# Kernel tuning notes

Hardware: AMD Instinct MI355X
Metric: run time of the kernel (lower is better)

Reference implementation:

```python
import jax, jax.numpy as jnp
import numpy as np

B, N, D, K, L, H, DFF = 2048, 64, 256, 32, 2, 8, 1024
TEMP = 10.0
EPS = 1e-10


def _ln(x, g, b):
    m = jnp.mean(x, -1, keepdims=True)
    v = jnp.mean((x - m) ** 2, -1, keepdims=True)
    return (x - m) * jax.lax.rsqrt(v + 1e-5) * g + b


def _mha(x, Wqkv, bqkv, Wo, bo):
    b, n, d = x.shape
    dh = d // H
    qkv = x @ Wqkv.T + bqkv                      # [b,n,3d]
    q, k, v = jnp.split(qkv, 3, axis=-1)
    q = q.reshape(b, n, H, dh)
    k = k.reshape(b, n, H, dh)
    v = v.reshape(b, n, H, dh)
    att = jnp.einsum('bqhd,bkhd->bhqk', q, k) / np.float32(np.sqrt(dh))
    att = jax.nn.softmax(att, axis=-1)
    o = jnp.einsum('bhqk,bkhd->bqhd', att, v).reshape(b, n, d)
    return o @ Wo.T + bo


def _encoder(x, Wqkv, bqkv, Wo, bo, ln1_g, ln1_b, ln2_g, ln2_b, W1, b1, W2, b2):
    # torch TransformerEncoder, norm_first=False (post-LN), dropout=0
    for l in range(L):
        x = _ln(x + _mha(x, Wqkv[l], bqkv[l], Wo[l], bo[l]), ln1_g[l], ln1_b[l])
        h = jax.nn.relu(x @ W1[l].T + b1[l]) @ W2[l].T + b2[l]
        x = _ln(x + h, ln2_g[l], ln2_b[l])
    return x


def _cluster_probs_from_emb(emb, mus):
    # ||x - tanh(mu)||^2 via expansion to avoid the [B,N,K,D] intermediate
    mt = jnp.tanh(mus)                                       # [K,D]
    d2 = (jnp.sum(emb ** 2, -1)[..., None]
          - 2.0 * jnp.einsum('bnd,kd->bnk', emb, mt)
          + jnp.sum(mt ** 2, -1))                            # [B,N,K]
    e = jnp.exp(-d2 / TEMP)
    return e / jnp.sum(e, -1, keepdims=True)


def _forward(input_series, init_logits, transition_logits,
             Wqkv, bqkv, Wo, bo, ln1_g, ln1_b, ln2_g, ln2_b,
             W1, b1, W2, b2, mus):
    prob_pi = jax.nn.softmax(init_logits, axis=0)            # [K]
    prob_A = jax.nn.softmax(transition_logits, axis=1)       # [K,K]
    emb_all = _encoder(input_series, Wqkv, bqkv, Wo, bo,
                       ln1_g, ln1_b, ln2_g, ln2_b, W1, b1, W2, b2)
    logits_all = _cluster_probs_from_emb(emb_all, mus)       # [B,N,K]

    log_emit = jnp.log(logits_all + EPS)                     # [B,N,K]
    lt0 = jax.nn.softmax(jnp.log(prob_pi + EPS)[None, :] + log_emit[:, 0], axis=1)

    def step(lt, le):
        lt = jax.nn.softmax(jnp.log(lt @ prob_A + EPS) + le, axis=1)
        return lt, lt

    _, rest = jax.lax.scan(step, lt0, jnp.swapaxes(log_emit[:, 1:], 0, 1))
    cluster_probs = jnp.concatenate([lt0[:, None], jnp.swapaxes(rest, 0, 1)], axis=1)
    entropy_loss = -jnp.mean(jnp.sum(cluster_probs * jnp.log(cluster_probs + EPS), -1))
    return cluster_probs, emb_all, prob_pi, prob_A, entropy_loss


def setup_inputs() -> dict:
    key = jax.random.key(0)
    ks = jax.random.split(key, 10)
    s = jnp.float32(0.02)
    return {
        'input_series': jax.random.normal(ks[0], (B, N, D), jnp.float32),
        'init_logits': jax.random.normal(ks[1], (K,), jnp.float32),
        'transition_logits': jax.random.normal(ks[2], (K, K), jnp.float32),
        'Wqkv': jax.random.normal(ks[3], (L, 3 * D, D), jnp.float32) * s,
        'bqkv': jnp.zeros((L, 3 * D), jnp.float32),
        'Wo': jax.random.normal(ks[4], (L, D, D), jnp.float32) * s,
        'bo': jnp.zeros((L, D), jnp.float32),
        'ln1_g': jnp.ones((L, D), jnp.float32),
        'ln1_b': jnp.zeros((L, D), jnp.float32),
        'ln2_g': jnp.ones((L, D), jnp.float32),
        'ln2_b': jnp.zeros((L, D), jnp.float32),
        'W1': jax.random.normal(ks[5], (L, DFF, D), jnp.float32) * s,
        'b1': jnp.zeros((L, DFF), jnp.float32),
        'W2': jax.random.normal(ks[6], (L, D, DFF), jnp.float32) * s,
        'b2': jnp.zeros((L, D), jnp.float32),
        'mus': jax.random.normal(ks[7], (K, D), jnp.float32),
    }


def reference(input_series, init_logits, transition_logits, Wqkv, bqkv, Wo, bo,
              ln1_g, ln1_b, ln2_g, ln2_b, W1, b1, W2, b2, mus):
    return _forward(input_series, init_logits, transition_logits, Wqkv, bqkv,
                    Wo, bo, ln1_g, ln1_b, ln2_g, ln2_b, W1, b1, W2, b2, mus)
```

## Files before the change

kernel.cpp:

```cpp
#include <hip/hip_runtime.h>

#define BB   2048
#define NNX  64
#define DD   256
#define KKC  32
#define LLN  2
#define HHN  8
#define DHH  32
#define DFFN 1024
#define BNT  (BB*NNX)

typedef short s16x8 __attribute__((ext_vector_type(8)));
typedef float f32x4 __attribute__((ext_vector_type(4)));

#define GLOAD_LDS16(gp, lp) __builtin_amdgcn_global_load_lds( \
    (const __attribute__((address_space(1))) void*)(gp),      \
    (__attribute__((address_space(3))) void*)(lp), 16, 0, 0)

#define WAITVM4() asm volatile("s_waitcnt vmcnt(4)" ::: "memory")
#define WAITVM0() asm volatile("s_waitcnt vmcnt(0)" ::: "memory")
#define WAITLGKM0() do { asm volatile("s_waitcnt lgkmcnt(0)" ::: "memory"); \
                         __builtin_amdgcn_sched_barrier(0); } while (0)
#define SBAR() __builtin_amdgcn_s_barrier()

__device__ __forceinline__ unsigned short f2bf(float f) {
  unsigned int u = __float_as_uint(f);
  u += 0x7fffu + ((u >> 16) & 1u);
  return (unsigned short)(u >> 16);
}
__device__ __forceinline__ float bf2f(unsigned short u) {
  return __uint_as_float(((unsigned int)u) << 16);
}

__device__ __forceinline__ unsigned char f2fp8(float f) {
  unsigned u = __float_as_uint(f);
  unsigned lsb = (u >> 20) & 1u;
  u += 0x7FFFFu + lsb;
  int e = (int)((u >> 23) & 255u) - 120;
  if (e <= 0) {
    int q = (int)(f * 512.f + 0.5f);
    return (unsigned char)q;
  }
  if (e > 15) return 0x7E;
  return (unsigned char)((e << 3) | ((u >> 20) & 7u));
}
__device__ __forceinline__ unsigned char f2fp8s(float f) {
  unsigned s = __float_as_uint(f) >> 31;
  float a = fminf(fabsf(f), 448.f);
  return (unsigned char)((s << 7) | f2fp8(a));
}
__device__ __forceinline__ unsigned char p2fp8(float f) {
  unsigned u = __float_as_uint(f);
  u += 0x7FFFFu + ((u >> 20) & 1u);
  int e = (int)((u >> 23) & 255u) - 120;
  if (e <= 0) return 0;
  return (unsigned char)((e << 3) | ((u >> 20) & 7u));
}

__global__ __launch_bounds__(256) void cvt_kernel(const float4* __restrict__ src,
                                                  ushort4* __restrict__ dst, int n4) {
  int i = blockIdx.x * 256 + threadIdx.x;
  int st = gridDim.x * 256;
  for (; i < n4; i += st) {
    float4 v = src[i];
    ushort4 o;
    o.x = f2bf(v.x); o.y = f2bf(v.y); o.z = f2bf(v.z); o.w = f2bf(v.w);
    dst[i] = o;
  }
}

__global__ __launch_bounds__(256) void cvtw_kernel(const float4* __restrict__ wq, ushort4* __restrict__ dq,
                                                   const float4* __restrict__ wo, ushort4* __restrict__ dov,
                                                   const float4* __restrict__ w1, ushort4* __restrict__ d1,
                                                   const float4* __restrict__ w2, uchar4* __restrict__ d2) {
  const int n0 = 98304, n1 = 32768, n2 = 131072, n3 = 131072;
  int i = blockIdx.x * 256 + threadIdx.x;
  int st = gridDim.x * 256;
  for (; i < n0 + n1 + n2 + n3; i += st) {
    int j = i;
    if (j < n0) {
      float4 v = wq[j];
      dq[j] = (ushort4){f2bf(v.x), f2bf(v.y), f2bf(v.z), f2bf(v.w)};
    } else if ((j -= n0) < n1) {
      float4 v = wo[j];
      dov[j] = (ushort4){f2bf(v.x), f2bf(v.y), f2bf(v.z), f2bf(v.w)};
    } else if ((j -= n1) < n2) {
      float4 v = w1[j];
      d1[j] = (ushort4){f2bf(v.x), f2bf(v.y), f2bf(v.z), f2bf(v.w)};
    } else {
      j -= n2;
      float4 v = w2[j];
      d2[j] = (uchar4){f2fp8s(v.x * 64.f), f2fp8s(v.y * 64.f),
                       f2fp8s(v.z * 64.f), f2fp8s(v.w * 64.f)};
    }
  }
}

__global__ void mtpi_kernel(const float* __restrict__ mus, unsigned short* __restrict__ mtb,
                            float* __restrict__ mtn,
                            const float* __restrict__ il, const float* __restrict__ tl,
                            float* __restrict__ d_pi, float* __restrict__ d_A,
                            float* __restrict__ d_ent) {
  int lane = threadIdx.x;
  if (blockIdx.x == 0) {
    if (lane < 32) {
      float acc = 0.f;
      for (int d = 0; d < 256; d++) {
        float t = tanhf(mus[lane * 256 + d]);
        mtb[lane * 264 + d] = f2bf(t);
        acc += t * t;
      }
      mtn[lane] = acc;
    }
  } else {
    if (lane == 0) *d_ent = 0.f;
    if (lane < 32) {
      float v = il[lane];
      float mx = v;
      #pragma unroll
      for (int off = 16; off; off >>= 1) mx = fmaxf(mx, __shfl_xor(mx, off, 32));
      float e = expf(v - mx), sm = e;
      #pragma unroll
      for (int off = 16; off; off >>= 1) sm += __shfl_xor(sm, off, 32);
      d_pi[lane] = e / sm;
      for (int r = 0; r < 32; r++) {
        float a = tl[r * 32 + lane];
        float m2 = a;
        #pragma unroll
        for (int off = 16; off; off >>= 1) m2 = fmaxf(m2, __shfl_xor(m2, off, 32));
        float e2 = expf(a - m2), s2 = e2;
        #pragma unroll
        for (int off = 16; off; off >>= 1) s2 += __shfl_xor(s2, off, 32);
        d_A[r * 32 + lane] = e2 / s2;
      }
    }
  }
}

template <int EPI>
__global__ __launch_bounds__(256, 4) void gemm_nt(const unsigned short* __restrict__ A,
                                                  const unsigned short* __restrict__ Bw,
                                                  const float* __restrict__ bias,
                                                  void* __restrict__ outp,
                                                  int N, int K, int nx) {
  __shared__ unsigned short lds[16384];
  const int t = threadIdx.x;
  const int bid = blockIdx.x, nwg = gridDim.x;
  const int wg = (bid & 7) * (nwg >> 3) + (bid >> 3);
  const int m0 = (wg / nx) << 7;
  const int n0 = (wg % nx) << 7;
  const int lane = t & 63, w = t >> 6;
  const int wm = w >> 1, wn = w & 1;
  const int lr = lane & 15, lk = lane >> 4;

  const int r0 = t >> 2, sg = t & 3;
  const int s0 = sg ^ ((r0 >> 1) & 3);
  const int r1 = r0 + 64;
  const int s1 = sg ^ ((r1 >> 1) & 3);
  const int aoff0 = (m0 + r0) * K + s0 * 8;
  const int aoff1 = (m0 + r1) * K + s1 * 8;
  const int boff0 = (n0 + r0) * K + s0 * 8;
  const int boff1 = (n0 + r1) * K + s1 * 8;

#define STAGE(buf, k0) do {                                    \
    char* la = (char*)lds + (buf) * 16384;                     \
    GLOAD_LDS16(A + aoff0 + (k0), la + t * 16);                \
    GLOAD_LDS16(A + aoff1 + (k0), la + 4096 + t * 16);         \
    GLOAD_LDS16(Bw + boff0 + (k0), la + 8192 + t * 16);        \
    GLOAD_LDS16(Bw + boff1 + (k0), la + 12288 + t * 16);       \
  } while (0)

  f32x4 acc[4][4];
  #pragma unroll
  for (int i = 0; i < 4; i++)
    #pragma unroll
    for (int j = 0; j < 4; j++) acc[i][j] = (f32x4)(0.f);

  const int ra = wm * 64 + lr, rb = wn * 64 + lr;
  const int sla = lk ^ ((ra >> 1) & 3), slb = lk ^ ((rb >> 1) & 3);

  const int NT = K >> 5;
  STAGE(0, 0);
  STAGE(1, 32);
  WAITVM4();
  SBAR();

  int c = 0;
  for (int kt = 0; kt < NT; kt++) {
    s16x8 af[4], bf[4];
    {
      const unsigned short* ua = lds + c * 8192;
      const unsigned short* ub = ua + 4096;
      #pragma unroll
      for (int mf = 0; mf < 4; mf++)
        af[mf] = *(const s16x8*)&ua[(ra + mf * 16) * 32 + sla * 8];
      #pragma unroll
      for (int nf = 0; nf < 4; nf++)
        bf[nf] = *(const s16x8*)&ub[(rb + nf * 16) * 32 + slb * 8];
    }
    __builtin_amdgcn_s_setprio(1);
    #pragma unroll
    for (int mf = 0; mf < 4; mf++)
      #pragma unroll
      for (int nf = 0; nf < 4; nf++)
        acc[mf][nf] = __builtin_amdgcn_mfma_f32_16x16x32_bf16(af[mf], bf[nf], acc[mf][nf], 0, 0, 0);
    __builtin_amdgcn_s_setprio(0);
    SBAR();
    if (kt < NT - 2) {
      STAGE(c, (kt + 2) << 5);
      WAITVM4();
    } else if (kt == NT - 2) {
      WAITVM0();
    }
    SBAR();
    c ^= 1;
  }
#undef STAGE

  #pragma unroll
  for (int nf = 0; nf < 4; nf++) {
    int col = n0 + wn * 64 + nf * 16 + lr;
    float bv = bias[col];
    #pragma unroll
    for (int mf = 0; mf < 4; mf++)
      #pragma unroll
      for (int r = 0; r < 4; r++) {
        int row = m0 + wm * 64 + mf * 16 + lk * 4 + r;
        size_t o = (size_t)row * N + col;
        float v = acc[mf][nf][r] + bv;
        if (EPI == 0) {
          ((unsigned short*)outp)[o] = f2bf(v);
        } else if (EPI == 1) {
          float hh = fminf(fmaxf(v, 0.f) * 8.f, 448.f);
          ((unsigned char*)outp)[o] = f2fp8(hh);
        } else {
          ((unsigned char*)outp)[o] = f2fp8s(v * 32.f);
        }
      }
  }
}

template <bool WR32>
__global__ __launch_bounds__(512) void gemm_ln(const unsigned short* __restrict__ A,
                                               const unsigned short* __restrict__ Bw,
                                               const float* __restrict__ bias,
                                               const unsigned short* __restrict__ res,
                                               const float* __restrict__ g,
                                               const float* __restrict__ bta,
                                               unsigned short* __restrict__ xb,
                                               float* __restrict__ x32,
                                               int K) {
  __shared__ unsigned short As[128 * 64];
  __shared__ unsigned short Bs[256 * 64];
  __shared__ float stats[2][128][4];
  const int t = threadIdx.x;
  const int nwg = gridDim.x;
  const int bid = blockIdx.x;
  const int wg = (bid & 7) * (nwg >> 3) + (bid >> 3);
  const int m0 = wg << 7;

  const int lane = t & 63, w = t >> 6;
  const int wm = w >> 2, wn = w & 3;
  const int lr = lane & 15, lk = lane >> 4;

  size_t aoff[2], boff[4];
  #pragma unroll
  for (int p = 0; p < 2; p++) {
    int u = p * 512 + t;
    int row = u >> 3, sp = u & 7;
    int seg = sp ^ (((row >> 2) & 1) << 1);
    aoff[p] = (size_t)(m0 + row) * K + seg * 8;
  }
  #pragma unroll
  for (int p = 0; p < 4; p++) {
    int u = p * 512 + t;
    int row = u >> 3, sp = u & 7;
    int seg = sp ^ (((row >> 2) & 1) << 1);
    boff[p] = (size_t)row * K + seg * 8;
  }

  f32x4 acc[4][4];
  #pragma unroll
  for (int i = 0; i < 4; i++)
    #pragma unroll
    for (int j = 0; j < 4; j++) acc[i][j] = (f32x4)(0.f);

  for (int k0 = 0; k0 < K; k0 += 64) {
    #pragma unroll
    for (int p = 0; p < 2; p++)
      GLOAD_LDS16(A + aoff[p] + k0, (char*)As + (p * 512 + t) * 16);
    #pragma unroll
    for (int p = 0; p < 4; p++)
      GLOAD_LDS16(Bw + boff[p] + k0, (char*)Bs + (p * 512 + t) * 16);
    __syncthreads();
    #pragma unroll
    for (int z = 0; z < 2; z++) {
      s16x8 af[4], bfr[4];
      #pragma unroll
      for (int mf = 0; mf < 4; mf++) {
        int row = wm * 64 + mf * 16 + lr;
        int cc = (z * 4 + lk) ^ (((row >> 2) & 1) << 1);
        af[mf] = *(const s16x8*)&As[row * 64 + cc * 8];
      }
      #pragma unroll
      for (int nf = 0; nf < 4; nf++) {
        int row = wn * 64 + nf * 16 + lr;
        int cc = (z * 4 + lk) ^ (((row >> 2) & 1) << 1);
        bfr[nf] = *(const s16x8*)&Bs[row * 64 + cc * 8];
      }
      #pragma unroll
      for (int mf = 0; mf < 4; mf++)
        #pragma unroll
        for (int nf = 0; nf < 4; nf++)
          acc[mf][nf] = __builtin_amdgcn_mfma_f32_16x16x32_bf16(af[mf], bfr[nf], acc[mf][nf], 0, 0, 0);
    }
    __syncthreads();
  }

  float bv[4];
  #pragma unroll
  for (int nf = 0; nf < 4; nf++) bv[nf] = bias[wn * 64 + nf * 16 + lr];

  #pragma unroll
  for (int mf = 0; mf < 4; mf++) {
    #pragma unroll
    for (int r = 0; r < 4; r++) {
      int grow = m0 + wm * 64 + mf * 16 + lk * 4 + r;
      float s = 0.f, q = 0.f;
      #pragma unroll
      for (int nf = 0; nf < 4; nf++) {
        int col = wn * 64 + nf * 16 + lr;
        float v = acc[mf][nf][r] + bv[nf] + bf2f(res[(size_t)grow * 256 + col]);
        acc[mf][nf][r] = v;
        s += v; q += v * v;
      }
      #pragma unroll
      for (int off = 1; off < 16; off <<= 1) { s += __shfl_xor(s, off); q += __shfl_xor(q, off); }
      if (lr == 0) {
        int lrow = wm * 64 + mf * 16 + lk * 4 + r;
        stats[0][lrow][wn] = s;
        stats[1][lrow][wn] = q;
      }
    }
  }
  __syncthreads();

  float gv[4], bbv[4];
  #pragma unroll
  for (int nf = 0; nf < 4; nf++) {
    int col = wn * 64 + nf * 16 + lr;
    gv[nf] = g[col]; bbv[nf] = bta[col];
  }
  #pragma unroll
  for (int mf = 0; mf < 4; mf++) {
    #pragma unroll
    for (int r = 0; r < 4; r++) {
      int lrow = wm * 64 + mf * 16 + lk * 4 + r;
      int grow = m0 + lrow;
      float s4 = stats[0][lrow][0] + stats[0][lrow][1] + stats[0][lrow][2] + stats[0][lrow][3];
      float q4 = stats[1][lrow][0] + stats[1][lrow][1] + stats[1][lrow][2] + stats[1][lrow][3];
      float mean = s4 * (1.f / 256.f);
      float var = q4 * (1.f / 256.f) - mean * mean;
      float rs = rsqrtf(var + 1e-5f);
      #pragma unroll
      for (int nf = 0; nf < 4; nf++) {
        int col = wn * 64 + nf * 16 + lr;
        float val = (acc[mf][nf][r] - mean) * rs * gv[nf] + bbv[nf];
        xb[(size_t)grow * 256 + col] = f2bf(val);
        if (WR32) x32[(size_t)grow * 256 + col] = val;
      }
    }
  }
}

template <bool WR32>
__global__ __launch_bounds__(512) void gemm_ln_fp8(const unsigned char* __restrict__ A,
                                                   const unsigned char* __restrict__ Bw,
                                                   const float* __restrict__ bias,
                                                   const unsigned short* __restrict__ res,
                                                   const float* __restrict__ g,
                                                   const float* __restrict__ bta,
                                                   unsigned short* __restrict__ xb,
                                                   float* __restrict__ x32,
                                                   int K) {
  __shared__ unsigned char lds8[24576];
  float* stats = (float*)lds8;
  const int t = threadIdx.x;
  const int nwg = gridDim.x;
  const int bid = blockIdx.x;
  const int wg = (bid & 7) * (nwg >> 3) + (bid >> 3);
  const int m0 = wg << 7;

  const int lane = t & 63, w = t >> 6;
  const int wm = w >> 2, wn = w & 3;
  const int lr = lane & 15, lk = lane >> 4;

  const int auu = t >> 8, arow = (t >> 1) & 127, asg = t & 1;
  const size_t aoff = (size_t)(m0 + arow) * K + auu * 32 + asg * 16;
  size_t boff[2];
  #pragma unroll
  for (int p = 0; p < 2; p++) {
    int idx = p * 512 + t;
    int buu = idx >> 9, brow = (idx >> 1) & 255, bsg = idx & 1;
    boff[p] = (size_t)brow * K + buu * 32 + bsg * 16;
  }

  f32x4 acc[4][4];
  #pragma unroll
  for (int i = 0; i < 4; i++)
    #pragma unroll
    for (int j = 0; j < 4; j++) acc[i][j] = (f32x4)(0.f);

  for (int k0 = 0; k0 < K; k0 += 64) {
    GLOAD_LDS16(A + aoff + k0, (char*)lds8 + t * 16);
    GLOAD_LDS16(Bw + boff[0] + k0, (char*)lds8 + 8192 + t * 16);
    GLOAD_LDS16(Bw + boff[1] + k0, (char*)lds8 + 16384 + t * 16);
    __syncthreads();
    #pragma unroll
    for (int kk = 0; kk < 2; kk++) {
      long long af[4], bf[4];
      #pragma unroll
      for (int mf = 0; mf < 4; mf++)
        af[mf] = *(const long long*)&lds8[kk * 4096 + (wm * 64 + mf * 16 + lr) * 32 + lk * 8];
      #pragma unroll
      for (int nf = 0; nf < 4; nf++)
        bf[nf] = *(const long long*)&lds8[8192 + kk * 8192 + (wn * 64 + nf * 16 + lr) * 32 + lk * 8];
      #pragma unroll
      for (int mf = 0; mf < 4; mf++)
        #pragma unroll
        for (int nf = 0; nf < 4; nf++)
          acc[mf][nf] = __builtin_amdgcn_mfma_f32_16x16x32_fp8_fp8(af[mf], bf[nf], acc[mf][nf], 0, 0, 0);
    }
    __syncthreads();
  }

  const float isc = 1.f / 512.f;
  float bv[4];
  #pragma unroll
  for (int nf = 0; nf < 4; nf++) bv[nf] = bias[wn * 64 + nf * 16 + lr];

  #pragma unroll
  for (int mf = 0; mf < 4; mf++) {
    #pragma unroll
    for (int r = 0; r < 4; r++) {
      int grow = m0 + wm * 64 + mf * 16 + lk * 4 + r;
      float s = 0.f, q = 0.f;
      #pragma unroll
      for (int nf = 0; nf < 4; nf++) {
        int col = wn * 64 + nf * 16 + lr;
        float v = acc[mf][nf][r] * isc + bv[nf] + bf2f(res[(size_t)grow * 256 + col]);
        acc[mf][nf][r] = v;
        s += v; q += v * v;
      }
      #pragma unroll
      for (int off = 1; off < 16; off <<= 1) { s += __shfl_xor(s, off); q += __shfl_xor(q, off); }
      if (lr == 0) {
        int lrow = wm * 64 + mf * 16 + lk * 4 + r;
        stats[lrow * 4 + wn] = s;
        stats[512 + lrow * 4 + wn] = q;
      }
    }
  }
  __syncthreads();

  float gv[4], bbv[4];
  #pragma unroll
  for (int nf = 0; nf < 4; nf++) {
    int col = wn * 64 + nf * 16 + lr;
    gv[nf] = g[col]; bbv[nf] = bta[col];
  }
  #pragma unroll
  for (int mf = 0; mf < 4; mf++) {
    #pragma unroll
    for (int r = 0; r < 4; r++) {
      int lrow = wm * 64 + mf * 16 + lk * 4 + r;
      int grow = m0 + lrow;
      float s4 = stats[lrow * 4 + 0] + stats[lrow * 4 + 1] + stats[lrow * 4 + 2] + stats[lrow * 4 + 3];
      float q4 = stats[512 + lrow * 4 + 0] + stats[512 + lrow * 4 + 1]
               + stats[512 + lrow * 4 + 2] + stats[512 + lrow * 4 + 3];
      float mean = s4 * (1.f / 256.f);
      float var = q4 * (1.f / 256.f) - mean * mean;
      float rs = rsqrtf(var + 1e-5f);
      #pragma unroll
      for (int nf = 0; nf < 4; nf++) {
        int col = wn * 64 + nf * 16 + lr;
        float val = (acc[mf][nf][r] - mean) * rs * gv[nf] + bbv[nf];
        xb[(size_t)grow * 256 + col] = f2bf(val);
        if (WR32) x32[(size_t)grow * 256 + col] = val;
      }
    }
  }
}

__global__ __launch_bounds__(64) void attn_kernel(const unsigned char* __restrict__ qkv,
                                                  unsigned short* __restrict__ ob) {
  __shared__ unsigned char al[7168];
  unsigned char* qs = al;
  unsigned char* ks = al + 2048;
  unsigned char* vs = al + 4096;
  unsigned char* vt = al;
  unsigned char* ps = al + 2304;
  const int bh = blockIdx.x;
  const int b = bh >> 3, h = bh & 7;
  const int lane = threadIdx.x;
  const int lr = lane & 15, lk = lane >> 4;

  #pragma unroll
  for (int p = 0; p < 2; p++) {
    int u = lane + p * 64;
    int row = u >> 1, seg = u & 1;
    size_t gb = (size_t)(b * 64 + row) * 768 + h * 32 + seg * 16;
    GLOAD_LDS16(qkv + gb, (char*)al + u * 16);
    GLOAD_LDS16(qkv + gb + 256, (char*)al + 2048 + u * 16);
    GLOAD_LDS16(qkv + gb + 512, (char*)al + 4096 + u * 16);
  }
  __syncthreads();

  long long aq[4], bk[4], vchunk[4];
  #pragma unroll
  for (int mi = 0; mi < 4; mi++)
    aq[mi] = *(const long long*)&qs[(mi * 16 + lr) * 32 + lk * 8];
  #pragma unroll
  for (int nj = 0; nj < 4; nj++)
    bk[nj] = *(const long long*)&ks[(nj * 16 + lr) * 32 + lk * 8];
  const int vrow = lane >> 2, vcs = (lane & 3) * 8;
  #pragma unroll
  for (int q = 0; q < 4; q++)
    vchunk[q] = *(const long long*)&vs[(q * 16 + vrow) * 32 + vcs];
  WAITLGKM0();

  #pragma unroll
  for (int q = 0; q < 4; q++) {
    unsigned long long vv = (unsigned long long)vchunk[q];
    #pragma unroll
    for (int j = 0; j < 8; j++)
      vt[(vcs + j) * 72 + q * 16 + vrow] = (unsigned char)(vv >> (8 * j));
  }

  f32x4 s[4][4];
  #pragma unroll
  for (int i = 0; i < 4; i++)
    #pragma unroll
    for (int j = 0; j < 4; j++) s[i][j] = (f32x4)(0.f);
  #pragma unroll
  for (int mi = 0; mi < 4; mi++)
    #pragma unroll
    for (int nj = 0; nj < 4; nj++)
      s[mi][nj] = __builtin_amdgcn_mfma_f32_16x16x32_fp8_fp8(aq[mi], bk[nj], s[mi][nj], 0, 0, 0);

  const float scale = 0.17677669529663687f / 1024.f;
  #pragma unroll
  for (int mi = 0; mi < 4; mi++) {
    #pragma unroll
    for (int r = 0; r < 4; r++) {
      float t0 = s[mi][0][r] * scale, t1 = s[mi][1][r] * scale;
      float t2 = s[mi][2][r] * scale, t3 = s[mi][3][r] * scale;
      float mx = fmaxf(fmaxf(t0, t1), fmaxf(t2, t3));
      #pragma unroll
      for (int off = 8; off; off >>= 1) mx = fmaxf(mx, __shfl_xor(mx, off, 16));
      float e0 = expf(t0 - mx), e1 = expf(t1 - mx), e2 = expf(t2 - mx), e3 = expf(t3 - mx);
      float sm = e0 + e1 + e2 + e3;
      #pragma unroll
      for (int off = 8; off; off >>= 1) sm += __shfl_xor(sm, off, 16);
      float inv = 128.f / sm;
      int prow = mi * 16 + lk * 4 + r;
      ps[prow * 72 + lr + 0]  = p2fp8(e0 * inv);
      ps[prow * 72 + lr + 16] = p2fp8(e1 * inv);
      ps[prow * 72 + lr + 32] = p2fp8(e2 * inv);
      ps[prow * 72 + lr + 48] = p2fp8(e3 * inv);
    }
  }
  WAITLGKM0();

  f32x4 oacc[4][2];
  #pragma unroll
  for (int i = 0; i < 4; i++) { oacc[i][0] = (f32x4)(0.f); oacc[i][1] = (f32x4)(0.f); }
  #pragma unroll
  for (int kk = 0; kk < 2; kk++) {
    long long bv[2];
    #pragma unroll
    for (int nf = 0; nf < 2; nf++)
      bv[nf] = *(const long long*)&vt[(nf * 16 + lr) * 72 + kk * 32 + lk * 8];
    #pragma unroll
    for (int mi = 0; mi < 4; mi++) {
      long long ap = *(const long long*)&ps[(mi * 16 + lr) * 72 + kk * 32 + lk * 8];
      #pragma unroll
      for (int nf = 0; nf < 2; nf++)
        oacc[mi][nf] = __builtin_amdgcn_mfma_f32_16x16x32_fp8_fp8(ap, bv[nf], oacc[mi][nf], 0, 0, 0);
    }
  }
  const float osc = 1.f / 4096.f;
  #pragma unroll
  for (int mi = 0; mi < 4; mi++)
    #pragma unroll
    for (int nf = 0; nf < 2; nf++)
      #pragma unroll
      for (int r = 0; r < 4; r++) {
        int tok = mi * 16 + lk * 4 + r;
        int c = nf * 16 + lr;
        ob[(size_t)(b * 64 + tok) * 256 + h * 32 + c] = f2bf(oacc[mi][nf][r] * osc);
      }
}

__global__ __launch_bounds__(256) void cluster_kernel(const unsigned short* __restrict__ xb,
                                                      const unsigned short* __restrict__ mtb,
                                                      const float* __restrict__ mtn,
                                                      float* __restrict__ log_emit) {
  __shared__ unsigned short ms[32 * 264];
  const int t = threadIdx.x;
  for (int i = t; i < 2112; i += 256)
    ((uint2*)ms)[i] = ((const uint2*)mtb)[i];
  const int lane = t & 63, w = t >> 6;
  const int lr = lane & 15, lk = lane >> 4;
  const float mtn0 = mtn[lr], mtn1 = mtn[16 + lr];
  __syncthreads();

  const size_t tok0 = (size_t)blockIdx.x * 256 + (size_t)w * 64;
  f32x4 s[4][2];
  #pragma unroll
  for (int i = 0; i < 4; i++) { s[i][0] = (f32x4)(0.f); s[i][1] = (f32x4)(0.f); }

  #pragma unroll
  for (int kk = 0; kk < 8; kk++) {
    s16x8 bf0 = *(const s16x8*)&ms[lr * 264 + lk * 8 + kk * 32];
    s16x8 bf1 = *(const s16x8*)&ms[(16 + lr) * 264 + lk * 8 + kk * 32];
    #pragma unroll
    for (int mi = 0; mi < 4; mi++) {
      s16x8 af = *(const s16x8*)&xb[(tok0 + mi * 16 + lr) * 256 + lk * 8 + kk * 32];
      s[mi][0] = __builtin_amdgcn_mfma_f32_16x16x32_bf16(af, bf0, s[mi][0], 0, 0, 0);
      s[mi][1] = __builtin_amdgcn_mfma_f32_16x16x32_bf16(af, bf1, s[mi][1], 0, 0, 0);
    }
  }

  #pragma unroll
  for (int mi = 0; mi < 4; mi++) {
    #pragma unroll
    for (int r = 0; r < 4; r++) {
      float l0 = (2.f * s[mi][0][r] - mtn0) * 0.1f;
      float l1 = (2.f * s[mi][1][r] - mtn1) * 0.1f;
      float mx = fmaxf(l0, l1);
      #pragma unroll
      for (int off = 8; off; off >>= 1) mx = fmaxf(mx, __shfl_xor(mx, off, 16));
      float e0 = expf(l0 - mx), e1 = expf(l1 - mx);
      float sm = e0 + e1;
      #pragma unroll
      for (int off = 8; off; off >>= 1) sm += __shfl_xor(sm, off, 16);
      float inv = 1.f / sm;
      size_t row = tok0 + mi * 16 + lk * 4 + r;
      log_emit[row * 32 + lr]      = logf(e0 * inv + 1e-10f);
      log_emit[row * 32 + 16 + lr] = logf(e1 * inv + 1e-10f);
    }
  }
}

__global__ __launch_bounds__(256) void scan_kernel(const float* __restrict__ log_emit,
                                                   const float* __restrict__ pi,
                                                   const float* __restrict__ A,
                                                   float* __restrict__ cp,
                                                   float* __restrict__ ent) {
  const int g = threadIdx.x >> 5, j = threadIdx.x & 31;
  const int batch = blockIdx.x * 8 + g;
  float regA[32];
  #pragma unroll
  for (int i = 0; i < 32; i++) regA[i] = A[i * 32 + j];
  const float* le = log_emit + (size_t)batch * 64 * 32;
  float* cpo = cp + (size_t)batch * 64 * 32;

  float u = logf(pi[j] + 1e-10f) + le[j];
  float mx = u;
  #pragma unroll
  for (int off = 16; off; off >>= 1) mx = fmaxf(mx, __shfl_xor(mx, off, 32));
  float e = expf(u - mx), sm = e;
  #pragma unroll
  for (int off = 16; off; off >>= 1) sm += __shfl_xor(sm, off, 32);
  float p = e / sm;
  cpo[j] = p;
  float enta = p * logf(p + 1e-10f);

  for (int n = 1; n < 64; n++) {
    float tt = 0.f;
    #pragma unroll
    for (int i = 0; i < 32; i++) tt += __shfl(p, i, 32) * regA[i];
    u = logf(tt + 1e-10f) + le[n * 32 + j];
    mx = u;
    #pragma unroll
    for (int off = 16; off; off >>= 1) mx = fmaxf(mx, __shfl_xor(mx, off, 32));
    e = expf(u - mx); sm = e;
    #pragma unroll
    for (int off = 16; off; off >>= 1) sm += __shfl_xor(sm, off, 32);
    p = e / sm;
    cpo[n * 32 + j] = p;
    enta += p * logf(p + 1e-10f);
  }
  #pragma unroll
  for (int off = 16; off; off >>= 1) enta += __shfl_xor(enta, off, 32);
  if (j == 0) atomicAdd(ent, -enta * (1.f / (2048.f * 64.f)));
}

extern "C" void kernel_launch(void* const* d_in, const int* in_sizes, int n_in,
                              void* d_out, int out_size, void* d_ws, size_t ws_size,
                              hipStream_t stream) {
  const float* input = (const float*)d_in[0];
  const float* init_logits = (const float*)d_in[1];
  const float* trans = (const float*)d_in[2];
  const float* Wqkv = (const float*)d_in[3];
  const float* bqkv = (const float*)d_in[4];
  const float* Wo = (const float*)d_in[5];
  const float* bo = (const float*)d_in[6];
  const float* ln1g = (const float*)d_in[7];
  const float* ln1b = (const float*)d_in[8];
  const float* ln2g = (const float*)d_in[9];
  const float* ln2b = (const float*)d_in[10];
  const float* W1 = (const float*)d_in[11];
  const float* b1 = (const float*)d_in[12];
  const float* W2 = (const float*)d_in[13];
  const float* b2 = (const float*)d_in[14];
  const float* mus = (const float*)d_in[15];

  float* out = (float*)d_out;
  float* cp = out;
  float* x = out + 4194304;
  float* d_pi = out + 37748736;
  float* d_A = out + 37748768;
  float* d_ent = out + 37749792;

  char* ws = (char*)d_ws;
  unsigned char* qkv = (unsigned char*)ws;
  unsigned char* hb = (unsigned char*)ws;
  float* log_emit = (float*)ws;
  unsigned short* ob = (unsigned short*)(ws + 268435456ull);
  unsigned short* xb = (unsigned short*)(ws + 335544320ull);
  unsigned short* wq_b = (unsigned short*)(ws + 402653184ull);
  unsigned short* wo_b = (unsigned short*)(ws + 402653184ull + 786432ull);
  unsigned short* w1_b = (unsigned short*)(ws + 402653184ull + 1048576ull);
  unsigned char* w2_f = (unsigned char*)(ws + 402653184ull + 2097152ull);
  unsigned short* mtb = (unsigned short*)(ws + 402653184ull + 3145728ull);
  float* mtn = (float*)(ws + 402653184ull + 3178496ull);

  cvt_kernel<<<2048, 256, 0, stream>>>((const float4*)input, (ushort4*)xb, BNT * 256 / 4);
  cvtw_kernel<<<512, 256, 0, stream>>>((const float4*)Wqkv, (ushort4*)wq_b,
                                       (const float4*)Wo, (ushort4*)wo_b,
                                       (const float4*)W1, (ushort4*)w1_b,
                                       (const float4*)W2, (uchar4*)w2_f);
  mtpi_kernel<<<2, 64, 0, stream>>>(mus, mtb, mtn, init_logits, trans, d_pi, d_A, d_ent);

  for (int l = 0; l < 2; l++) {
    gemm_nt<2><<<6144, 256, 0, stream>>>(xb, wq_b + l * 196608, bqkv + l * 768,
                                         qkv, 768, 256, 6);
    attn_kernel<<<16384, 64, 0, stream>>>(qkv, ob);
    gemm_ln<false><<<1024, 512, 0, stream>>>(ob, wo_b + l * 65536, bo + l * 256,
                                             xb, ln1g + l * 256, ln1b + l * 256,
                                             xb, nullptr, 256);
    gemm_nt<1><<<8192, 256, 0, stream>>>(xb, w1_b + l * 262144, b1 + l * 1024,
                                         hb, 1024, 256, 8);
    if (l == LLN - 1)
      gemm_ln_fp8<true><<<1024, 512, 0, stream>>>(hb, w2_f + l * 262144, b2 + l * 256,
                                                  xb, ln2g + l * 256, ln2b + l * 256,
                                                  xb, x, 1024);
    else
      gemm_ln_fp8<false><<<1024, 512, 0, stream>>>(hb, w2_f + l * 262144, b2 + l * 256,
                                                   xb, ln2g + l * 256, ln2b + l * 256,
                                                   xb, nullptr, 1024);
  }

  cluster_kernel<<<512, 256, 0, stream>>>(xb, mtb, mtn, log_emit);
  scan_kernel<<<256, 256, 0, stream>>>(log_emit, d_pi, d_A, cp, d_ent);
}
```

Before: 1.075 ms.

## Fuse cluster and scan kernels, merge setup kernels, pack four attention heads per block

```diff
diff --git a/kernel.cpp b/kernel.cpp
--- a/kernel.cpp
+++ b/kernel.cpp
@@ -72,10 +72,52 @@
 __global__ __launch_bounds__(256) void cvtw_kernel(const float4* __restrict__ wq, ushort4* __restrict__ dq,
                                                    const float4* __restrict__ wo, ushort4* __restrict__ dov,
                                                    const float4* __restrict__ w1, ushort4* __restrict__ d1,
-                                                   const float4* __restrict__ w2, uchar4* __restrict__ d2) {
+                                                   const float4* __restrict__ w2, uchar4* __restrict__ d2,
+                                                   const float* __restrict__ mus, unsigned short* __restrict__ mtb,
+                                                   float* __restrict__ mtn,
+                                                   const float* __restrict__ il, const float* __restrict__ tl,
+                                                   float* __restrict__ d_pi, float* __restrict__ d_A,
+                                                   float* __restrict__ d_ent) {
+  if (blockIdx.x >= 512) {
+    int lane = threadIdx.x;
+    if (blockIdx.x == 512) {
+      if (lane < 32) {
+        float acc = 0.f;
+        for (int d = 0; d < 256; d++) {
+          float t = tanhf(mus[lane * 256 + d]);
+          mtb[lane * 264 + d] = f2bf(t);
+          acc += t * t;
+        }
+        mtn[lane] = acc;
+      }
+    } else {
+      if (lane == 0) *d_ent = 0.f;
+      if (lane < 32) {
+        float v = il[lane];
+        float mx = v;
+        #pragma unroll
+        for (int off = 16; off; off >>= 1) mx = fmaxf(mx, __shfl_xor(mx, off, 32));
+        float e = expf(v - mx), sm = e;
+        #pragma unroll
+        for (int off = 16; off; off >>= 1) sm += __shfl_xor(sm, off, 32);
+        d_pi[lane] = e / sm;
+        for (int r = 0; r < 32; r++) {
+          float a = tl[r * 32 + lane];
+          float m2 = a;
+          #pragma unroll
+          for (int off = 16; off; off >>= 1) m2 = fmaxf(m2, __shfl_xor(m2, off, 32));
+          float e2 = expf(a - m2), s2 = e2;
+          #pragma unroll
+          for (int off = 16; off; off >>= 1) s2 += __shfl_xor(s2, off, 32);
+          d_A[r * 32 + lane] = e2 / s2;
+        }
+      }
+    }
+    return;
+  }
   const int n0 = 98304, n1 = 32768, n2 = 131072, n3 = 131072;
   int i = blockIdx.x * 256 + threadIdx.x;
-  int st = gridDim.x * 256;
+  int st = 512 * 256;
   for (; i < n0 + n1 + n2 + n3; i += st) {
     int j = i;
     if (j < n0) {
@@ -92,47 +134,6 @@
       float4 v = w2[j];
       d2[j] = (uchar4){f2fp8s(v.x * 64.f), f2fp8s(v.y * 64.f),
                        f2fp8s(v.z * 64.f), f2fp8s(v.w * 64.f)};
-    }
-  }
-}
-
-__global__ void mtpi_kernel(const float* __restrict__ mus, unsigned short* __restrict__ mtb,
-                            float* __restrict__ mtn,
-                            const float* __restrict__ il, const float* __restrict__ tl,
-                            float* __restrict__ d_pi, float* __restrict__ d_A,
-                            float* __restrict__ d_ent) {
-  int lane = threadIdx.x;
-  if (blockIdx.x == 0) {
-    if (lane < 32) {
-      float acc = 0.f;
-      for (int d = 0; d < 256; d++) {
-        float t = tanhf(mus[lane * 256 + d]);
-        mtb[lane * 264 + d] = f2bf(t);
-        acc += t * t;
-      }
-      mtn[lane] = acc;
-    }
-  } else {
-    if (lane == 0) *d_ent = 0.f;
-    if (lane < 32) {
-      float v = il[lane];
-      float mx = v;
-      #pragma unroll
-      for (int off = 16; off; off >>= 1) mx = fmaxf(mx, __shfl_xor(mx, off, 32));
-      float e = expf(v - mx), sm = e;
-      #pragma unroll
-      for (int off = 16; off; off >>= 1) sm += __shfl_xor(sm, off, 32);
-      d_pi[lane] = e / sm;
-      for (int r = 0; r < 32; r++) {
-        float a = tl[r * 32 + lane];
-        float m2 = a;
-        #pragma unroll
-        for (int off = 16; off; off >>= 1) m2 = fmaxf(m2, __shfl_xor(m2, off, 32));
-        float e2 = expf(a - m2), s2 = e2;
-        #pragma unroll
-        for (int off = 16; off; off >>= 1) s2 += __shfl_xor(s2, off, 32);
-        d_A[r * 32 + lane] = e2 / s2;
-      }
     }
   }
 }
@@ -492,17 +493,19 @@
   }
 }
 
-__global__ __launch_bounds__(64) void attn_kernel(const unsigned char* __restrict__ qkv,
-                                                  unsigned short* __restrict__ ob) {
-  __shared__ unsigned char al[7168];
-  unsigned char* qs = al;
-  unsigned char* ks = al + 2048;
-  unsigned char* vs = al + 4096;
-  unsigned char* vt = al;
-  unsigned char* ps = al + 2304;
-  const int bh = blockIdx.x;
+__global__ __launch_bounds__(256) void attn_kernel(const unsigned char* __restrict__ qkv,
+                                                   unsigned short* __restrict__ ob) {
+  __shared__ unsigned char al[28672];
+  const int wv = threadIdx.x >> 6;
+  unsigned char* wb = al + wv * 7168;
+  unsigned char* qs = wb;
+  unsigned char* ks = wb + 2048;
+  unsigned char* vs = wb + 4096;
+  unsigned char* vt = wb;
+  unsigned char* ps = wb + 2304;
+  const int bh = blockIdx.x * 4 + wv;
   const int b = bh >> 3, h = bh & 7;
-  const int lane = threadIdx.x;
+  const int lane = threadIdx.x & 63;
   const int lr = lane & 15, lk = lane >> 4;
 
   #pragma unroll
@@ -510,9 +513,9 @@
     int u = lane + p * 64;
     int row = u >> 1, seg = u & 1;
     size_t gb = (size_t)(b * 64 + row) * 768 + h * 32 + seg * 16;
-    GLOAD_LDS16(qkv + gb, (char*)al + u * 16);
-    GLOAD_LDS16(qkv + gb + 256, (char*)al + 2048 + u * 16);
-    GLOAD_LDS16(qkv + gb + 512, (char*)al + 4096 + u * 16);
+    GLOAD_LDS16(qkv + gb, (char*)wb + u * 16);
+    GLOAD_LDS16(qkv + gb + 256, (char*)wb + 2048 + u * 16);
+    GLOAD_LDS16(qkv + gb + 512, (char*)wb + 4096 + u * 16);
   }
   __syncthreads();
 
@@ -602,11 +605,15 @@
       }
 }
 
-__global__ __launch_bounds__(256) void cluster_kernel(const unsigned short* __restrict__ xb,
-                                                      const unsigned short* __restrict__ mtb,
-                                                      const float* __restrict__ mtn,
-                                                      float* __restrict__ log_emit) {
+__global__ __launch_bounds__(256) void cluster_scan_kernel(const unsigned short* __restrict__ xb,
+                                                           const unsigned short* __restrict__ mtb,
+                                                           const float* __restrict__ mtn,
+                                                           const float* __restrict__ pi,
+                                                           const float* __restrict__ Atr,
+                                                           float* __restrict__ cp,
+                                                           float* __restrict__ ent) {
   __shared__ unsigned short ms[32 * 264];
+  __shared__ float les[4][64][32];
   const int t = threadIdx.x;
   for (int i = t; i < 2112; i += 256)
     ((uint2*)ms)[i] = ((const uint2*)mtb)[i];
@@ -646,55 +653,50 @@
       #pragma unroll
       for (int off = 8; off; off >>= 1) sm += __shfl_xor(sm, off, 16);
       float inv = 1.f / sm;
-      size_t row = tok0 + mi * 16 + lk * 4 + r;
-      log_emit[row * 32 + lr]      = logf(e0 * inv + 1e-10f);
-      log_emit[row * 32 + 16 + lr] = logf(e1 * inv + 1e-10f);
-    }
-  }
-}
-
-__global__ __launch_bounds__(256) void scan_kernel(const float* __restrict__ log_emit,
-                                                   const float* __restrict__ pi,
-                                                   const float* __restrict__ A,
-                                                   float* __restrict__ cp,
-                                                   float* __restrict__ ent) {
-  const int g = threadIdx.x >> 5, j = threadIdx.x & 31;
-  const int batch = blockIdx.x * 8 + g;
-  float regA[32];
-  #pragma unroll
-  for (int i = 0; i < 32; i++) regA[i] = A[i * 32 + j];
-  const float* le = log_emit + (size_t)batch * 64 * 32;
-  float* cpo = cp + (size_t)batch * 64 * 32;
-
-  float u = logf(pi[j] + 1e-10f) + le[j];
-  float mx = u;
-  #pragma unroll
-  for (int off = 16; off; off >>= 1) mx = fmaxf(mx, __shfl_xor(mx, off, 32));
-  float e = expf(u - mx), sm = e;
-  #pragma unroll
-  for (int off = 16; off; off >>= 1) sm += __shfl_xor(sm, off, 32);
-  float p = e / sm;
-  cpo[j] = p;
-  float enta = p * logf(p + 1e-10f);
-
-  for (int n = 1; n < 64; n++) {
-    float tt = 0.f;
-    #pragma unroll
-    for (int i = 0; i < 32; i++) tt += __shfl(p, i, 32) * regA[i];
-    u = logf(tt + 1e-10f) + le[n * 32 + j];
-    mx = u;
+      int row = mi * 16 + lk * 4 + r;
+      les[w][row][lr]      = logf(e0 * inv + 1e-10f);
+      les[w][row][16 + lr] = logf(e1 * inv + 1e-10f);
+    }
+  }
+
+  if (lane < 32) {
+    const int j = lane;
+    const int batch = blockIdx.x * 4 + w;
+    float regA[32];
+    #pragma unroll
+    for (int i = 0; i < 32; i++) regA[i] = Atr[i * 32 + j];
+    float* cpo = cp + (size_t)batch * 64 * 32;
+
+    float u = logf(pi[j] + 1e-10f) + les[w][0][j];
+    float mx = u;
     #pragma unroll
     for (int off = 16; off; off >>= 1) mx = fmaxf(mx, __shfl_xor(mx, off, 32));
-    e = expf(u - mx); sm = e;
+    float e = expf(u - mx), sm = e;
     #pragma unroll
     for (int off = 16; off; off >>= 1) sm += __shfl_xor(sm, off, 32);
-    p = e / sm;
-    cpo[n * 32 + j] = p;
-    enta += p * logf(p + 1e-10f);
-  }
-  #pragma unroll
-  for (int off = 16; off; off >>= 1) enta += __shfl_xor(enta, off, 32);
-  if (j == 0) atomicAdd(ent, -enta * (1.f / (2048.f * 64.f)));
+    float p = e / sm;
+    cpo[j] = p;
+    float enta = p * logf(p + 1e-10f);
+
+    for (int n = 1; n < 64; n++) {
+      float tt = 0.f;
+      #pragma unroll
+      for (int i = 0; i < 32; i++) tt += __shfl(p, i, 32) * regA[i];
+      u = logf(tt + 1e-10f) + les[w][n][j];
+      mx = u;
+      #pragma unroll
+      for (int off = 16; off; off >>= 1) mx = fmaxf(mx, __shfl_xor(mx, off, 32));
+      e = expf(u - mx); sm = e;
+      #pragma unroll
+      for (int off = 16; off; off >>= 1) sm += __shfl_xor(sm, off, 32);
+      p = e / sm;
+      cpo[n * 32 + j] = p;
+      enta += p * logf(p + 1e-10f);
+    }
+    #pragma unroll
+    for (int off = 16; off; off >>= 1) enta += __shfl_xor(enta, off, 32);
+    if (j == 0) atomicAdd(ent, -enta * (1.f / (2048.f * 64.f)));
+  }
 }
 
 extern "C" void kernel_launch(void* const* d_in, const int* in_sizes, int n_in,
@@ -727,7 +729,6 @@
   char* ws = (char*)d_ws;
   unsigned char* qkv = (unsigned char*)ws;
   unsigned char* hb = (unsigned char*)ws;
-  float* log_emit = (float*)ws;
   unsigned short* ob = (unsigned short*)(ws + 268435456ull);
   unsigned short* xb = (unsigned short*)(ws + 335544320ull);
   unsigned short* wq_b = (unsigned short*)(ws + 402653184ull);
@@ -738,16 +739,17 @@
   float* mtn = (float*)(ws + 402653184ull + 3178496ull);
 
   cvt_kernel<<<2048, 256, 0, stream>>>((const float4*)input, (ushort4*)xb, BNT * 256 / 4);
-  cvtw_kernel<<<512, 256, 0, stream>>>((const float4*)Wqkv, (ushort4*)wq_b,
+  cvtw_kernel<<<514, 256, 0, stream>>>((const float4*)Wqkv, (ushort4*)wq_b,
                                        (const float4*)Wo, (ushort4*)wo_b,
                                        (const float4*)W1, (ushort4*)w1_b,
-                                       (const float4*)W2, (uchar4*)w2_f);
-  mtpi_kernel<<<2, 64, 0, stream>>>(mus, mtb, mtn, init_logits, trans, d_pi, d_A, d_ent);
+                                       (const float4*)W2, (uchar4*)w2_f,
+                                       mus, mtb, mtn,
+                                       init_logits, trans, d_pi, d_A, d_ent);
 
   for (int l = 0; l < 2; l++) {
     gemm_nt<2><<<6144, 256, 0, stream>>>(xb, wq_b + l * 196608, bqkv + l * 768,
                                          qkv, 768, 256, 6);
-    attn_kernel<<<16384, 64, 0, stream>>>(qkv, ob);
+    attn_kernel<<<4096, 256, 0, stream>>>(qkv, ob);
     gemm_ln<false><<<1024, 512, 0, stream>>>(ob, wo_b + l * 65536, bo + l * 256,
                                              xb, ln1g + l * 256, ln1b + l * 256,
                                              xb, nullptr, 256);
@@ -763,6 +765,5 @@
                                                    xb, nullptr, 1024);
   }
 
-  cluster_kernel<<<512, 256, 0, stream>>>(xb, mtb, mtn, log_emit);
-  scan_kernel<<<256, 256, 0, stream>>>(log_emit, d_pi, d_A, cp, d_ent);
-}
+  cluster_scan_kernel<<<512, 256, 0, stream>>>(xb, mtb, mtn, d_pi, d_A, cp, d_ent);
+}
```

Measured after the change: 1.060 ms (median of 2 runs). Within noise of the previous version (-1.4%).
